# Performance work log

Hardware: AMD Instinct MI355X
Metric: run time of the kernel (lower is better)

The kernel has to match this reference:

```python
import jax, jax.numpy as jnp
import numpy as np

G, B, T, H = 14, 64, 2048, 6  # nb_gaussians, batch, track_len, nb_hidden_variables
LOG_2PI = float(np.log(2.0 * np.pi))


def _dnn(x, d):
    # tf.math.divide_no_nan, safe under autodiff
    d_safe = jnp.where(d == 0, 1.0, d)
    return jnp.where(d == 0, 0.0, x / d_safe)


def _norm_log_gaussian(t):
    return -0.5 * (LOG_2PI + t ** 2)


def _gaussian_product(c1, c2, n1, n2, b1, b2, k):
    # RNN_gaussian_product: combine gaussians 1,2 so output-3 no longer depends
    # on coef k and output-4 carries it. (Tiny 1e-20/1e-100 TF noise terms are
    # numerically void and omitted.)
    C1 = c1[:, :, k:k + 1]  # [B,T,1]
    C2 = c2[:, :, k:k + 1]
    cc1, cc2 = _dnn(c1, C1), _dnn(c2, C2)
    nn1, nn2 = _dnn(n1, C1), _dnn(n2, C2)
    bb1, bb2 = _dnn(b1, C1[:, :, 0]), _dnn(b2, C2[:, :, 0])
    var1 = 1.0 / C1 ** 2
    var2 = 1.0 / C2 ** 2
    var3 = var1 + var2
    std3 = jnp.sqrt(var3)
    c3 = (cc1 - cc2) / std3
    n3 = (nn1 - nn2) / std3
    b3 = (bb1 - bb2) / std3[:, :, 0]
    var4 = var1 * var2 / var3
    std4 = jnp.sqrt(var4)
    den = var3 * std4
    c4 = (cc1 * var2 + cc2 * var1) / den
    n4 = (nn1 * var2 + nn2 * var1) / den
    b4 = (bb1 * var2[:, :, 0] + bb2 * var1[:, :, 0]) / den[:, :, 0]
    logC = -jnp.log(jnp.abs(C1 * C2 * std4 * std3))[:, :, 0]
    return logC, c3, c4, n3, n4, b3, b4


def _forward(cur, nxt, biases):
    nH = cur.shape[-1]
    cur_l = list(cur)
    nxt_l = list(nxt)
    b_l = list(biases)
    LC = jnp.zeros(cur.shape[1:3], cur.dtype)  # [B,T]
    # Phase 1: integrate out each current hidden variable k.
    for k in range(nH):
        n = len(b_l)
        for i in range(n - 1):
            logC, c3, c4, n3, n4, b3, b4 = _gaussian_product(
                cur_l[i], cur_l[i + 1], nxt_l[i], nxt_l[i + 1], b_l[i], b_l[i + 1], k)
            cur_l[i], cur_l[i + 1] = c3, c4
            nxt_l[i], nxt_l[i + 1] = n3, n4
            b_l[i], b_l[i + 1] = b3, b4
            LC = LC + logC
        # final_RNN_function_phase_1: integrate & drop last dependent gaussian
        LC = LC - jnp.log(jnp.abs(cur_l[n - 1][:, :, k]))
        cur_l.pop(n - 1)
        nxt_l.pop(n - 1)
        b_l.pop(n - 1)
    # Phase 2: roles of current/next swapped; pop dependent gaussian into kept.
    kept_n, kept_b = [], []
    for k in range(nH):
        n = len(b_l)
        for i in range(n - 1):
            logC, n3, n4, c3, c4, b3, b4 = _gaussian_product(
                nxt_l[i], nxt_l[i + 1], cur_l[i], cur_l[i + 1], b_l[i], b_l[i + 1], k)
            nxt_l[i], nxt_l[i + 1] = n3, n4
            cur_l[i], cur_l[i + 1] = c3, c4
            b_l[i], b_l[i + 1] = b3, b4
            LC = LC + logC
        kept_n.append(nxt_l.pop(n - 1))
        kept_b.append(b_l.pop(n - 1))
        cur_l.pop(n - 1)
    # Remaining gaussians are pure constants
    LC = LC + jnp.sum(_norm_log_gaussian(jnp.stack(b_l)), axis=0)
    return jnp.stack(kept_n), jnp.stack(kept_b), LC


def setup_inputs() -> dict:
    key = jax.random.key(0)
    ks = jax.random.split(key, 5)

    def coefs(k1, k2, shape):
        mag = jax.random.uniform(k1, shape, jnp.float32, 0.5, 1.5)
        sgn = jnp.where(jax.random.bernoulli(k2, 0.5, shape), 1.0, -1.0)
        return mag * sgn

    cur = coefs(ks[0], ks[1], (G, B, T, H))
    nxt = coefs(ks[2], ks[3], (G, B, T, H))
    biases = jax.random.normal(ks[4], (G, B, T), jnp.float32)
    return {"current_hidden_var_coefs": cur,
            "next_hidden_var_coefs": nxt,
            "biases": biases}


def reference(current_hidden_var_coefs, next_hidden_var_coefs, biases):
    return _forward(current_hidden_var_coefs, next_hidden_var_coefs, biases)
```

## Files before the change

### kernel.cpp

```cpp
#include <hip/hip_runtime.h>

#define Gc 14
#define Hc 6
#define NPc (64*2048)
#define LOG_2PI 1.8378770664093453f

typedef float v2f __attribute__((ext_vector_type(2)));

__device__ __forceinline__ float frsq(float x){ return __builtin_amdgcn_rsqf(x); }

__device__ __forceinline__ v2f pk_mul(v2f a, v2f b){
    v2f d; asm("v_pk_mul_f32 %0, %1, %2" : "=v"(d) : "v"(a), "v"(b)); return d;
}
__device__ __forceinline__ v2f pk_fma(v2f a, v2f b, v2f c){
    v2f d; asm("v_pk_fma_f32 %0, %1, %2, %3" : "=v"(d) : "v"(a), "v"(b), "v"(c)); return d;
}

template<int CTRL>
__device__ __forceinline__ float dppf(float x){
    union { float f; int i; } u; u.f = x;
    u.i = __builtin_amdgcn_update_dpp(0, u.i, CTRL, 0xF, 0xF, true);
    return u.f;
}
template<int OQ>
__device__ __forceinline__ float bcast(float x){
    return (OQ == 0) ? dppf<0xA0>(x) : dppf<0xF5>(x);
}

__device__ __forceinline__ void nt_store_v2f(float* p, v2f v){
    union { v2f f; unsigned long long u; } c; c.f = v;
    __builtin_nontemporal_store(c.u, (unsigned long long*)p);
}

template<int J, int C, int N, int OQ>
__device__ __forceinline__ void sweep(v2f (&st)[Gc][3], float (&bb)[Gc]){
#pragma unroll
    for (int i = 0; i < N - 1; ++i){
        const float C1 = bcast<OQ>(st[i][J][C]);
        const float C2 = bcast<OQ>(st[i + 1][J][C]);
        const float S  = frsq(fmaf(C1, C1, C2 * C2));
        const float s1 = C2 * S, s2 = C1 * S;
        const float a1 = copysignf(s1, C1), a2n = -copysignf(s2, C2);
        const v2f A1 = {a1, a1}, A2N = {a2n, a2n}, S1 = {s1, s1}, S2 = {s2, s2};
#pragma unroll
        for (int j = 0; j < 3; ++j){
            const v2f x = st[i][j], y = st[i + 1][j];
            st[i][j]     = pk_fma(x, A1, pk_mul(y, A2N));
            st[i + 1][j] = pk_fma(x, S2, pk_mul(y, S1));
        }
        {
            const float x = bb[i], y = bb[i + 1];
            bb[i]     = fmaf(x, a1, y * a2n);
            bb[i + 1] = fmaf(x, s2, y * s1);
        }
    }
}

__global__ void __launch_bounds__(256, 2)
gaussmerge_kernel(const float* __restrict__ cur_in,
                  const float* __restrict__ nxt_in,
                  const float* __restrict__ b_in,
                  float* __restrict__ out)
{
    const int tid = threadIdx.x;
    const int q = tid & 1;
    const int p = blockIdx.x * 128 + (tid >> 1);

    v2f   st[Gc][3];
    float bb[Gc];

    const float* abase = (q ? nxt_in : cur_in) + (size_t)p * Hc;
    const float* bp    = b_in + p;
#pragma unroll
    for (int g = 0; g < Gc; ++g){
        const float* rec = abase + (size_t)g * (NPc * Hc);
        const float4 A = *(const float4*)rec;
        const float2 B = *(const float2*)(rec + 4);
        st[g][0] = (v2f){A.x, A.y};
        st[g][1] = (v2f){A.z, A.w};
        st[g][2] = (v2f){B.x, B.y};
        bb[g] = bp[(size_t)g * NPc];
    }

    float LC = 0.0f;

    sweep<0, 0, 14, 0>(st, bb); LC -= __logf(fabsf(st[13][0][0]));
    sweep<0, 1, 13, 0>(st, bb); LC -= __logf(fabsf(st[12][0][1]));
    sweep<1, 0, 12, 0>(st, bb); LC -= __logf(fabsf(st[11][1][0]));
    sweep<1, 1, 11, 0>(st, bb); LC -= __logf(fabsf(st[10][1][1]));
    sweep<2, 0, 10, 0>(st, bb); LC -= __logf(fabsf(st[ 9][2][0]));
    sweep<2, 1,  9, 0>(st, bb); LC -= __logf(fabsf(st[ 8][2][1]));

    float* outN = out;
    float* outB = out + (size_t)Hc * NPc * Hc;
    float* outL = outB + (size_t)Hc * NPc;

#define PH2(K, J, C, N)                                                         \
    sweep<J, C, N, 1>(st, bb);                                                  \
    {                                                                           \
        constexpr int m = 7 - (K);                                              \
        if (q) {                                                                \
            float* o = outN + (size_t)(K) * (NPc * Hc) + (size_t)p * Hc;        \
            nt_store_v2f(o,     st[m][0]);                                      \
            nt_store_v2f(o + 2, st[m][1]);                                      \
            nt_store_v2f(o + 4, st[m][2]);                                      \
        } else {                                                                \
            __builtin_nontemporal_store(bb[m], outB + (size_t)(K) * NPc + p);   \
        }                                                                       \
    }

    PH2(0, 0, 0, 8)
    PH2(1, 0, 1, 7)
    PH2(2, 1, 0, 6)
    PH2(3, 1, 1, 5)
    PH2(4, 2, 0, 4)
    PH2(5, 2, 1, 3)
#undef PH2

    LC += -0.5f * (LOG_2PI + bb[0] * bb[0]);
    LC += -0.5f * (LOG_2PI + bb[1] * bb[1]);
    if (q == 0) __builtin_nontemporal_store(LC, outL + p);
}

extern "C" void kernel_launch(void* const* d_in, const int* in_sizes, int n_in,
                              void* d_out, int out_size, void* d_ws, size_t ws_size,
                              hipStream_t stream) {
    const float* cur = (const float*)d_in[0];
    const float* nxt = (const float*)d_in[1];
    const float* bia = (const float*)d_in[2];
    float* out = (float*)d_out;

    dim3 grid((NPc * 2) / 256), block(256);
    gaussmerge_kernel<<<grid, block, 0, stream>>>(cur, nxt, bia, out);
}
```

Before: 31.50 us.

## Split each point across four lanes instead of two, folding bias into lane state

Each point's work now spans a quad of four lanes instead of a pair. Lanes 0-1 hold current coefficients and lanes 2-3 hold next coefficients, and the bias is carried as a duplicated pair in the odd lanes in place of a separate scalar array. Per-thread register state shrinks from 42+14 floats to 28 floats, so launch bounds are raised to 4 blocks per SIMD and the grid doubles. The aim is higher occupancy and shorter dependent chains. In exchange the rotation-coefficient math is repeated across more lanes, loads become narrower 8-byte accesses, and some lanes do redundant bias arithmetic.

```diff
diff --git a/kernel.cpp b/kernel.cpp
--- a/kernel.cpp
+++ b/kernel.cpp
@@ -22,104 +22,99 @@
     u.i = __builtin_amdgcn_update_dpp(0, u.i, CTRL, 0xF, 0xF, true);
     return u.f;
 }
-template<int OQ>
-__device__ __forceinline__ float bcast(float x){
-    return (OQ == 0) ? dppf<0xA0>(x) : dppf<0xF5>(x);
-}
+template<int L>
+__device__ __forceinline__ float qbcast(float x){ return dppf<L * 0x55>(x); }
 
 __device__ __forceinline__ void nt_store_v2f(float* p, v2f v){
     union { v2f f; unsigned long long u; } c; c.f = v;
     __builtin_nontemporal_store(c.u, (unsigned long long*)p);
 }
 
-template<int J, int C, int N, int OQ>
-__device__ __forceinline__ void sweep(v2f (&st)[Gc][3], float (&bb)[Gc]){
+template<int L, int B, int C, int N>
+__device__ __forceinline__ void sweep(v2f (&st)[Gc][2]){
 #pragma unroll
     for (int i = 0; i < N - 1; ++i){
-        const float C1 = bcast<OQ>(st[i][J][C]);
-        const float C2 = bcast<OQ>(st[i + 1][J][C]);
+        const float C1 = qbcast<L>(st[i][B][C]);
+        const float C2 = qbcast<L>(st[i + 1][B][C]);
         const float S  = frsq(fmaf(C1, C1, C2 * C2));
         const float s1 = C2 * S, s2 = C1 * S;
         const float a1 = copysignf(s1, C1), a2n = -copysignf(s2, C2);
         const v2f A1 = {a1, a1}, A2N = {a2n, a2n}, S1 = {s1, s1}, S2 = {s2, s2};
 #pragma unroll
-        for (int j = 0; j < 3; ++j){
+        for (int j = 0; j < 2; ++j){
             const v2f x = st[i][j], y = st[i + 1][j];
             st[i][j]     = pk_fma(x, A1, pk_mul(y, A2N));
             st[i + 1][j] = pk_fma(x, S2, pk_mul(y, S1));
         }
-        {
-            const float x = bb[i], y = bb[i + 1];
-            bb[i]     = fmaf(x, a1, y * a2n);
-            bb[i + 1] = fmaf(x, s2, y * s1);
-        }
     }
 }
 
-__global__ void __launch_bounds__(256, 2)
+__global__ void __launch_bounds__(256, 4)
 gaussmerge_kernel(const float* __restrict__ cur_in,
                   const float* __restrict__ nxt_in,
                   const float* __restrict__ b_in,
                   float* __restrict__ out)
 {
     const int tid = threadIdx.x;
-    const int q = tid & 1;
-    const int p = blockIdx.x * 128 + (tid >> 1);
+    const int l = tid & 3;
+    const int p = blockIdx.x * 64 + (tid >> 2);
 
-    v2f   st[Gc][3];
-    float bb[Gc];
+    const float* arr   = (l < 2) ? cur_in : nxt_in;
+    const float* baseA = arr + (size_t)p * Hc + ((l & 1) ? 2 : 0);
+    const float* baseB = arr + (size_t)p * Hc + 4;
+    const float* bp    = b_in + p;
 
-    const float* abase = (q ? nxt_in : cur_in) + (size_t)p * Hc;
-    const float* bp    = b_in + p;
+    v2f st[Gc][2];
 #pragma unroll
     for (int g = 0; g < Gc; ++g){
-        const float* rec = abase + (size_t)g * (NPc * Hc);
-        const float4 A = *(const float4*)rec;
-        const float2 B = *(const float2*)(rec + 4);
-        st[g][0] = (v2f){A.x, A.y};
-        st[g][1] = (v2f){A.z, A.w};
-        st[g][2] = (v2f){B.x, B.y};
-        bb[g] = bp[(size_t)g * NPc];
+        const v2f A = *(const v2f*)(baseA + (size_t)g * (NPc * Hc));
+        const v2f M = *(const v2f*)(baseB + (size_t)g * (NPc * Hc));
+        const float bv = bp[(size_t)g * NPc];
+        st[g][0] = A;
+        st[g][1] = (l & 1) ? (v2f){bv, bv} : M;
     }
 
     float LC = 0.0f;
 
-    sweep<0, 0, 14, 0>(st, bb); LC -= __logf(fabsf(st[13][0][0]));
-    sweep<0, 1, 13, 0>(st, bb); LC -= __logf(fabsf(st[12][0][1]));
-    sweep<1, 0, 12, 0>(st, bb); LC -= __logf(fabsf(st[11][1][0]));
-    sweep<1, 1, 11, 0>(st, bb); LC -= __logf(fabsf(st[10][1][1]));
-    sweep<2, 0, 10, 0>(st, bb); LC -= __logf(fabsf(st[ 9][2][0]));
-    sweep<2, 1,  9, 0>(st, bb); LC -= __logf(fabsf(st[ 8][2][1]));
+    sweep<0, 0, 0, 14>(st); LC -= __logf(fabsf(qbcast<0>(st[13][0][0])));
+    sweep<0, 0, 1, 13>(st); LC -= __logf(fabsf(qbcast<0>(st[12][0][1])));
+    sweep<1, 0, 0, 12>(st); LC -= __logf(fabsf(qbcast<1>(st[11][0][0])));
+    sweep<1, 0, 1, 11>(st); LC -= __logf(fabsf(qbcast<1>(st[10][0][1])));
+    sweep<0, 1, 0, 10>(st); LC -= __logf(fabsf(qbcast<0>(st[ 9][1][0])));
+    sweep<0, 1, 1,  9>(st); LC -= __logf(fabsf(qbcast<0>(st[ 8][1][1])));
 
     float* outN = out;
     float* outB = out + (size_t)Hc * NPc * Hc;
     float* outL = outB + (size_t)Hc * NPc;
 
-#define PH2(K, J, C, N)                                                         \
-    sweep<J, C, N, 1>(st, bb);                                                  \
+#define PH2(K, L_, B_, C_, N_)                                                  \
+    sweep<L_, B_, C_, N_>(st);                                                  \
     {                                                                           \
         constexpr int m = 7 - (K);                                              \
-        if (q) {                                                                \
-            float* o = outN + (size_t)(K) * (NPc * Hc) + (size_t)p * Hc;        \
-            nt_store_v2f(o,     st[m][0]);                                      \
-            nt_store_v2f(o + 2, st[m][1]);                                      \
-            nt_store_v2f(o + 4, st[m][2]);                                      \
-        } else {                                                                \
-            __builtin_nontemporal_store(bb[m], outB + (size_t)(K) * NPc + p);   \
+        float* o = outN + (size_t)(K) * (NPc * Hc) + (size_t)p * Hc;            \
+        if (l == 2){                                                            \
+            nt_store_v2f(o,     st[m][0]);                        \
+            nt_store_v2f(o + 4, st[m][1]);                        \
+        } else if (l == 3){                                                     \
+            nt_store_v2f(o + 2, st[m][0]);                        \
+        } else if (l == 1){                                                     \
+            __builtin_nontemporal_store(st[m][1][0], outB + (size_t)(K) * NPc + p); \
         }                                                                       \
     }
 
-    PH2(0, 0, 0, 8)
-    PH2(1, 0, 1, 7)
-    PH2(2, 1, 0, 6)
-    PH2(3, 1, 1, 5)
-    PH2(4, 2, 0, 4)
-    PH2(5, 2, 1, 3)
+    PH2(0, 2, 0, 0, 8)
+    PH2(1, 2, 0, 1, 7)
+    PH2(2, 3, 0, 0, 6)
+    PH2(3, 3, 0, 1, 5)
+    PH2(4, 2, 1, 0, 4)
+    PH2(5, 2, 1, 1, 3)
 #undef PH2
 
-    LC += -0.5f * (LOG_2PI + bb[0] * bb[0]);
-    LC += -0.5f * (LOG_2PI + bb[1] * bb[1]);
-    if (q == 0) __builtin_nontemporal_store(LC, outL + p);
+    const float b0 = qbcast<1>(st[0][1][0]);
+    const float b1 = qbcast<1>(st[1][1][0]);
+    LC += -0.5f * (LOG_2PI + b0 * b0);
+    LC += -0.5f * (LOG_2PI + b1 * b1);
+    if (l == 0) __builtin_nontemporal_store(LC, outL + p);
 }
 
 extern "C" void kernel_launch(void* const* d_in, const int* in_sizes, int n_in,
@@ -130,6 +125,6 @@
     const float* bia = (const float*)d_in[2];
     float* out = (float*)d_out;
 
-    dim3 grid((NPc * 2) / 256), block(256);
+    dim3 grid((NPc * 4) / 256), block(256);
     gaussmerge_kernel<<<grid, block, 0, stream>>>(cur, nxt, bia, out);
 }
```

Result: slower. 41.73 us (+32.5%).
